# Kernel tuning notes

Hardware: AMD Instinct MI355X
Metric: run time of the kernel (lower is better)

Reference implementation:

```python
import jax, jax.numpy as jnp
import numpy as np

B, L, V, N = 2, 2048, 32000, 1024  # batch, seq, vocab, n_embd (ambient dim = N+1)


def _sanitize(x):
    return jnp.nan_to_num(x, nan=0.0, posinf=1e4, neginf=-1e4)


def _safe_acosh(x):
    # safe_acosh_v2: Taylor expansion near x=1 to avoid gradient explosion.
    xm1 = jnp.maximum(x - 1.0, 0.0)
    near = xm1 < 1e-3
    taylor = jnp.sqrt(2.0 * jnp.maximum(xm1, 1e-12)) * (1.0 - xm1 / 12.0)
    exact = jnp.arccosh(jnp.maximum(x, 1.0 + 1e-7))
    return jnp.where(near, taylor, exact)


def setup_inputs() -> dict:
    key = jax.random.key(0)
    k1, k2 = jax.random.split(key)
    # Build valid Lorentz points on H^n: x0 = sqrt(1 + ||x_spatial||^2)
    sp = 0.5 * jax.random.normal(k1, (B, L, N), dtype=jnp.float32)
    t = jnp.sqrt(1.0 + jnp.sum(sp * sp, axis=-1, keepdims=True))
    hidden_states = jnp.concatenate([t, sp], axis=-1)  # [B, L, N+1]
    weight = 0.01 * jax.random.normal(k2, (V, N), dtype=jnp.float32)  # tangent vectors
    logit_scale = jnp.asarray(1.0 / np.sqrt(N), dtype=jnp.float32)  # init_logit_scale/sqrt(n_embd)
    return {"hidden_states": hidden_states, "weight": weight, "logit_scale": logit_scale}


def reference(hidden_states, weight, logit_scale):
    h = _sanitize(hidden_states)
    # exp_map_zero of zero-padded tangent vectors [V, N] -> hyperboloid points [V, N+1]
    # exp_o(v) = cosh(||v||) * o + sinh(||v||)/||v|| * v, with o = (1, 0, ..., 0)
    norm = jnp.linalg.norm(weight, axis=-1)  # [V]
    r = jnp.where(norm > 1e-7, jnp.sinh(norm) / jnp.maximum(norm, 1e-7), 1.0)
    w_time = jnp.cosh(norm)          # [V]
    w_space = r[:, None] * weight    # [V, N]
    # Lorentz distance: d = acosh(-<h, w>_L), -<h,w>_L = h0*w0 - h_sp . w_sp
    # Expressed as a GEMM over the vocab instead of a [B,L,V,N+1] broadcast.
    x = h[..., :1] * w_time[None, None, :] - jnp.einsum('bln,vn->blv', h[..., 1:], w_space)
    d = _safe_acosh(x)  # [B, L, V]
    tau = jnp.clip(logit_scale, 0.01, 2.5)
    logits = -tau * d * d
    return _sanitize(logits)
```

## Files before the change

kernel.cpp:

```cpp
#include <hip/hip_runtime.h>
#include <hip/hip_bf16.h>
#include <hip/hip_fp8.h>
#include <math.h>

#define M_TOT 4096
#define K_TOT 1024
#define V_TOT 32000

typedef int int4v __attribute__((ext_vector_type(4)));
typedef int int8v __attribute__((ext_vector_type(8)));
typedef float f32x4 __attribute__((ext_vector_type(4)));

__device__ __forceinline__ void gload_lds16(const void* g, void* l) {
  __builtin_amdgcn_global_load_lds(
      (const __attribute__((address_space(1))) void*)g,
      (__attribute__((address_space(3))) void*)l, 16, 0, 0);
}

__device__ __forceinline__ float sani(float v) {
  return (v != v) ? 0.0f : fminf(fmaxf(v, -1e4f), 1e4f);
}

__device__ __forceinline__ int pk4_fp8(float a, float b, float c, float d) {
#if __has_builtin(__builtin_amdgcn_cvt_pk_fp8_f32)
  int p = __builtin_amdgcn_cvt_pk_fp8_f32(a, b, 0, false);
  p = __builtin_amdgcn_cvt_pk_fp8_f32(c, d, p, true);
  return p;
#else
  union { unsigned char b4[4]; int i; } u;
  u.b4[0] = __hip_fp8_e4m3(a).__x;
  u.b4[1] = __hip_fp8_e4m3(b).__x;
  u.b4[2] = __hip_fp8_e4m3(c).__x;
  u.b4[3] = __hip_fp8_e4m3(d).__x;
  return u.i;
#endif
}

__global__ void prep_hw(const float* __restrict__ h, const float* __restrict__ w,
                        unsigned char* __restrict__ h8, unsigned char* __restrict__ w8,
                        float* __restrict__ h0, float* __restrict__ wtime) {
  __shared__ float red[4];
  __shared__ float r_sh;
  const int b = blockIdx.x;
  const int t = threadIdx.x;
  if (b < M_TOT) {
    const int m = b;
    const float* row = h + (long)m * (K_TOT + 1);
    if (t == 0) h0[m] = sani(row[0]);
    float4 x = *(const float4*)(row + 1 + t * 4);
    ((int*)(h8 + (long)m * K_TOT))[t] =
        pk4_fp8(sani(x.x), sani(x.y), sani(x.z), sani(x.w));
  } else {
    const int v = b - M_TOT;
    const float* row = w + (long)v * K_TOT;
    float4 x = *(const float4*)(row + t * 4);
    float s = x.x * x.x + x.y * x.y + x.z * x.z + x.w * x.w;
#pragma unroll
    for (int off = 32; off > 0; off >>= 1) s += __shfl_down(s, off);
    int lane = t & 63, wv = t >> 6;
    if (lane == 0) red[wv] = s;
    __syncthreads();
    if (t == 0) {
      float tot = red[0] + red[1] + red[2] + red[3];
      float norm = sqrtf(tot);
      float r = (norm > 1e-7f) ? (sinhf(norm) / fmaxf(norm, 1e-7f)) : 1.0f;
      r_sh = r;
      wtime[v] = coshf(norm);
    }
    __syncthreads();
    float sc = 16.0f * r_sh;
    ((int*)(w8 + (long)v * K_TOT))[t] =
        pk4_fp8(sc * x.x, sc * x.y, sc * x.z, sc * x.w);
  }
}

#define BAR __builtin_amdgcn_s_barrier()
#define LGKM0 asm volatile("s_waitcnt lgkmcnt(0)" ::: "memory")
#define VM4 asm volatile("s_waitcnt vmcnt(4)" ::: "memory")

__global__ __launch_bounds__(256, 2) void gemm_geo(
    const unsigned char* __restrict__ h8, const unsigned char* __restrict__ w8,
    const float* __restrict__ h0, const float* __restrict__ wtime,
    const float* __restrict__ ls, float* __restrict__ out) {
  __shared__ __align__(16) char smem[65536];

  const int t = threadIdx.x;
  const int wave = t >> 6, lane = t & 63;
  const int fr = lane & 15, fq = lane >> 4;
  const int wm = wave >> 1, wn = wave & 1;

  const int bid = blockIdx.x;
  const int swz = (bid & 7) * 500 + (bid >> 3);
  const int g = swz >> 4;
  const int sub = swz & 15;
  const int half = (g >= 125) ? 1 : 0;
  const int tile_v = g - half * 125;
  const int tile_m = half * 16 + sub;
  const int row0 = tile_m * 128;
  const int col0 = tile_v * 256;

  const int xorv = fr & 7;
  const int c0 = ((2 * fq) ^ xorv) * 16;
  const int c1 = ((2 * fq + 1) ^ xorv) * 16;
  const int a_rd = (wm * 64 + fr) * 128;
  const int b_rd = 32768 + (wn * 128 + fr) * 128;

  auto RDF = [&](int off) -> int8v {
    int4v lo = *(const int4v*)(smem + off + c0);
    int4v hi = *(const int4v*)(smem + off + c1);
    return (int8v){lo[0], lo[1], lo[2], lo[3], hi[0], hi[1], hi[2], hi[3]};
  };

  const int cc = (t & 7) ^ ((t >> 3) & 7);
  const unsigned char* pA = h8 + ((long)row0 + (t >> 3)) * K_TOT + cc * 16;
  const unsigned char* pB = w8 + ((long)col0 + (t >> 3)) * K_TOT + cc * 16;
  const int dst_w = wave * 1024;

  auto STAGE_A = [&](int kt, int bufo) {
#pragma unroll
    for (int hh = 0; hh < 4; ++hh)
      gload_lds16(pA + (long)hh * (32L * K_TOT) + kt * 128,
                  smem + bufo + hh * 4096 + dst_w);
  };
  auto STAGE_B = [&](int kt) {
#pragma unroll
    for (int hh = 0; hh < 8; ++hh)
      gload_lds16(pB + (long)hh * (32L * K_TOT) + kt * 128,
                  smem + 32768 + hh * 4096 + dst_w);
  };

  f32x4 acc[4][8];
#pragma unroll
  for (int i = 0; i < 4; ++i)
#pragma unroll
    for (int j = 0; j < 8; ++j) acc[i][j] = (f32x4)(0.0f);

  STAGE_A(0, 0);
  STAGE_B(0);
  STAGE_A(1, 16384);
  VM4;
  BAR;

#pragma unroll 1
  for (int kt = 0; kt < 8; ++kt) {
    const int cbo = (kt & 1) << 14;
    const int skB = (kt + 1 < 8) ? kt + 1 : 7;
    const int skA = (kt + 2 < 8) ? kt + 2 : 7;

    int8v bv[8], av[4];
#pragma unroll
    for (int iv = 0; iv < 8; ++iv) bv[iv] = RDF(b_rd + iv * 2048);
#pragma unroll
    for (int im = 0; im < 4; ++im) av[im] = RDF(cbo + a_rd + im * 2048);
    LGKM0;
    __builtin_amdgcn_sched_barrier(0);
    BAR;

    STAGE_B(skB);
    STAGE_A(skA, cbo);

    __builtin_amdgcn_s_setprio(1);
#pragma unroll
    for (int im = 0; im < 4; ++im)
#pragma unroll
      for (int iv = 0; iv < 8; ++iv)
        acc[im][iv] = __builtin_amdgcn_mfma_scale_f32_16x16x128_f8f6f4(
            bv[iv], av[im], acc[im][iv], 0, 0, 0, 0x7B7B7B7B, 0, 0x7F7F7F7F);
    __builtin_amdgcn_s_setprio(0);

    VM4;
    BAR;
  }

  const float ntau = -fminf(fmaxf(ls[0], 0.01f), 2.5f);
  const float LN2 = 0.69314718055994531f;
  f32x4 wt4[8];
#pragma unroll
  for (int iv = 0; iv < 8; ++iv)
    wt4[iv] = *(const f32x4*)&wtime[col0 + wn * 128 + iv * 16 + fq * 4];
#pragma unroll
  for (int im = 0; im < 4; ++im) {
    const float hh = h0[row0 + wm * 64 + im * 16 + fr];
    float* orow = out + (long)(row0 + wm * 64 + im * 16 + fr) * V_TOT + col0 +
                  wn * 128;
    f32x4 rv[8];
#pragma unroll
    for (int iv = 0; iv < 8; ++iv) {
#pragma unroll
      for (int j = 0; j < 4; ++j) {
        float x = fmaf(hh, wt4[iv][j], -acc[im][iv][j]);
        float xm1 = fmaxf(x - 1.0f, 0.0f);
        float arg = fmaxf(fmaf(x, x, -1.0f), 0.0f);
        float lg2 = __builtin_amdgcn_logf(x + __builtin_amdgcn_sqrtf(arg));
        float dex = LN2 * lg2;
        float d2_exact = dex * dex;
        float ts = fmaf(xm1, -1.0f / 12.0f, 1.0f);
        float d2_tay = 2.0f * xm1 * ts * ts;
        float d2 = (xm1 < 1e-3f) ? d2_tay : d2_exact;
        rv[iv][j] = ntau * d2;
      }
    }
#pragma unroll
    for (int iv = 0; iv < 8; ++iv)
      __builtin_nontemporal_store(rv[iv], (f32x4*)(orow + iv * 16 + fq * 4));
  }
}

extern "C" void kernel_launch(void* const* d_in, const int* in_sizes, int n_in,
                              void* d_out, int out_size, void* d_ws, size_t ws_size,
                              hipStream_t stream) {
  const float* h = (const float*)d_in[0];
  const float* w = (const float*)d_in[1];
  const float* ls = (const float*)d_in[2];
  float* out = (float*)d_out;

  char* ws = (char*)d_ws;
  unsigned char* w8 = (unsigned char*)ws;
  unsigned char* h8 = (unsigned char*)(ws + 32768000);
  float* wtime = (float*)(ws + 32768000 + 4194304);
  float* h0 = (float*)(ws + 32768000 + 4194304 + 128000);

  prep_hw<<<M_TOT + V_TOT, 256, 0, stream>>>(h, w, h8, w8, h0, wtime);
  gemm_geo<<<4000, 256, 0, stream>>>(h8, w8, h0, wtime, ls, out);
}
```

Before: 268.0 us.

## Load A fragments directly into registers and double-buffer B in LDS

Result: slower. 273.8 us (+2.2%).

```diff
diff --git a/kernel.cpp b/kernel.cpp
--- a/kernel.cpp
+++ b/kernel.cpp
@@ -75,8 +75,7 @@
 }
 
 #define BAR __builtin_amdgcn_s_barrier()
-#define LGKM0 asm volatile("s_waitcnt lgkmcnt(0)" ::: "memory")
-#define VM4 asm volatile("s_waitcnt vmcnt(4)" ::: "memory")
+#define VM8 asm volatile("s_waitcnt vmcnt(8)" ::: "memory")
 
 __global__ __launch_bounds__(256, 2) void gemm_geo(
     const unsigned char* __restrict__ h8, const unsigned char* __restrict__ w8,
@@ -102,8 +101,7 @@
   const int xorv = fr & 7;
   const int c0 = ((2 * fq) ^ xorv) * 16;
   const int c1 = ((2 * fq + 1) ^ xorv) * 16;
-  const int a_rd = (wm * 64 + fr) * 128;
-  const int b_rd = 32768 + (wn * 128 + fr) * 128;
+  const int b_rd = (wn * 128 + fr) * 128;
 
   auto RDF = [&](int off) -> int8v {
     int4v lo = *(const int4v*)(smem + off + c0);
@@ -112,22 +110,22 @@
   };
 
   const int cc = (t & 7) ^ ((t >> 3) & 7);
-  const unsigned char* pA = h8 + ((long)row0 + (t >> 3)) * K_TOT + cc * 16;
   const unsigned char* pB = w8 + ((long)col0 + (t >> 3)) * K_TOT + cc * 16;
   const int dst_w = wave * 1024;
 
-  auto STAGE_A = [&](int kt, int bufo) {
-#pragma unroll
-    for (int hh = 0; hh < 4; ++hh)
-      gload_lds16(pA + (long)hh * (32L * K_TOT) + kt * 128,
+  auto STAGE_B = [&](int kt, int bufo) {
+#pragma unroll
+    for (int hh = 0; hh < 8; ++hh)
+      gload_lds16(pB + (long)hh * (32L * K_TOT) + kt * 128,
                   smem + bufo + hh * 4096 + dst_w);
   };
-  auto STAGE_B = [&](int kt) {
-#pragma unroll
-    for (int hh = 0; hh < 8; ++hh)
-      gload_lds16(pB + (long)hh * (32L * K_TOT) + kt * 128,
-                  smem + 32768 + hh * 4096 + dst_w);
-  };
+
+  const unsigned char* pA0 =
+      h8 + ((long)row0 + wm * 64 + fr) * K_TOT + fq * 32;
+  const unsigned char* pAv0 = pA0;
+  const unsigned char* pAv1 = pA0 + 16L * K_TOT;
+  const unsigned char* pAv2 = pA0 + 32L * K_TOT;
+  const unsigned char* pAv3 = pA0 + 48L * K_TOT;
 
   f32x4 acc[4][8];
 #pragma unroll
@@ -135,41 +133,43 @@
 #pragma unroll
     for (int j = 0; j < 8; ++j) acc[i][j] = (f32x4)(0.0f);
 
-  STAGE_A(0, 0);
-  STAGE_B(0);
-  STAGE_A(1, 16384);
-  VM4;
-  BAR;
+  STAGE_B(0, 0);
 
 #pragma unroll 1
   for (int kt = 0; kt < 8; ++kt) {
-    const int cbo = (kt & 1) << 14;
+    const int cbo = (kt & 1) << 15;
+    const int nbo = cbo ^ 32768;
     const int skB = (kt + 1 < 8) ? kt + 1 : 7;
-    const int skA = (kt + 2 < 8) ? kt + 2 : 7;
-
-    int8v bv[8], av[4];
-#pragma unroll
-    for (int iv = 0; iv < 8; ++iv) bv[iv] = RDF(b_rd + iv * 2048);
-#pragma unroll
-    for (int im = 0; im < 4; ++im) av[im] = RDF(cbo + a_rd + im * 2048);
-    LGKM0;
-    __builtin_amdgcn_sched_barrier(0);
+    const int ko = kt * 128;
+
+    int4v alo[4], ahi[4];
+    alo[0] = *(const int4v*)(pAv0 + ko); ahi[0] = *(const int4v*)(pAv0 + ko + 16);
+    alo[1] = *(const int4v*)(pAv1 + ko); ahi[1] = *(const int4v*)(pAv1 + ko + 16);
+    alo[2] = *(const int4v*)(pAv2 + ko); ahi[2] = *(const int4v*)(pAv2 + ko + 16);
+    alo[3] = *(const int4v*)(pAv3 + ko); ahi[3] = *(const int4v*)(pAv3 + ko + 16);
+
+    VM8;
     BAR;
 
-    STAGE_B(skB);
-    STAGE_A(skA, cbo);
+    STAGE_B(skB, nbo);
+
+    int8v bv[8];
+#pragma unroll
+    for (int iv = 0; iv < 8; ++iv) bv[iv] = RDF(cbo + b_rd + iv * 2048);
+
+    VM8;
 
     __builtin_amdgcn_s_setprio(1);
 #pragma unroll
-    for (int im = 0; im < 4; ++im)
+    for (int im = 0; im < 4; ++im) {
+      int8v av = (int8v){alo[im][0], alo[im][1], alo[im][2], alo[im][3],
+                         ahi[im][0], ahi[im][1], ahi[im][2], ahi[im][3]};
 #pragma unroll
       for (int iv = 0; iv < 8; ++iv)
         acc[im][iv] = __builtin_amdgcn_mfma_scale_f32_16x16x128_f8f6f4(
-            bv[iv], av[im], acc[im][iv], 0, 0, 0, 0x7B7B7B7B, 0, 0x7F7F7F7F);
+            bv[iv], av, acc[im][iv], 0, 0, 0, 0x7B7B7B7B, 0, 0x7F7F7F7F);
+    }
     __builtin_amdgcn_s_setprio(0);
-
-    VM4;
-    BAR;
   }
 
   const float ntau = -fminf(fmaxf(ls[0], 0.01f), 2.5f);
```
